# Optimization experiments

Hardware: AMD Instinct MI355X
Metric: run time of the kernel (lower is better)

Reference implementation:

```python
import jax, jax.numpy as jnp
import numpy as np
import math

B, T, C = 4, 2048, 1024
H = 16  # parallelAttentionPathways
D = C // H  # head dim = 64


def setup_inputs() -> dict:
    key = jax.random.key(0)
    k1, k2, k3 = jax.random.split(key, 3)
    x = jax.random.normal(k1, (B, T, C), dtype=jnp.float32)
    w_qkv = jax.random.normal(k2, (3 * C, C), dtype=jnp.float32) * (1.0 / math.sqrt(C))
    w_out = jax.random.normal(k3, (C, C), dtype=jnp.float32) * (1.0 / math.sqrt(C))
    return {"x": x, "w_qkv": w_qkv, "w_out": w_out}


def reference(x, w_qkv, w_out):
    b, t, c = x.shape
    # qkv projection: torch Linear y = x @ W^T (no bias)
    qkv = jnp.einsum('btc,fc->btf', x, w_qkv)  # [B,T,3C]
    q, k, v = jnp.split(qkv, 3, axis=-1)
    # [B,H,T,D]
    q = q.reshape(b, t, H, D).transpose(0, 2, 1, 3)
    k = k.reshape(b, t, H, D).transpose(0, 2, 1, 3)
    v = v.reshape(b, t, H, D).transpose(0, 2, 1, 3)
    scale = 1.0 / math.sqrt(D)
    att = jnp.einsum('bhqd,bhkd->bhqk', q, k) * scale  # [B,H,T,T]
    causal = jnp.tril(jnp.ones((t, t), dtype=bool))
    att = jnp.where(causal[None, None], att, -jnp.inf)
    att = jax.nn.softmax(att, axis=-1)
    # dropoutRate=0.0 -> dropout is identity (eval-mode determinism)
    y = jnp.einsum('bhqk,bhkd->bhqd', att, v)  # [B,H,T,D]
    y = y.transpose(0, 2, 1, 3).reshape(b, t, c)
    return jnp.einsum('btc,fc->btf', y, w_out)
```

## Files before the change

kernel.cpp:

```cpp
#include <hip/hip_runtime.h>
#include <hip/hip_bf16.h>
#include <stdint.h>


using bf16 = __hip_bfloat16;
typedef __attribute__((ext_vector_type(8))) __bf16 bf16x8;
typedef __attribute__((ext_vector_type(8))) unsigned short u16x8;
typedef __attribute__((ext_vector_type(4))) unsigned short u16x4;
typedef __attribute__((ext_vector_type(4))) float f32x4;
typedef unsigned short ushort_t;

#define MFMA16(a, b, c) __builtin_amdgcn_mfma_f32_16x16x32_bf16((a), (b), (c), 0, 0, 0)

__device__ __forceinline__ bf16x8 ld_frag(const ushort_t* p) {
  const u16x8 u = *(const u16x8*)p;
  return __builtin_bit_cast(bf16x8, u);
}

__device__ __forceinline__ ushort_t f2bf(float f) {
  return __builtin_bit_cast(ushort_t, __float2bfloat16(f));
}

__device__ __forceinline__ void gl2lds16(const void* g, void* lds) {
  __builtin_amdgcn_global_load_lds((const __attribute__((address_space(1))) void*)g,
                                   (__attribute__((address_space(3))) void*)lds,
                                   16, 0, 0);
}

__global__ void detect_dtype(const ushort_t* __restrict__ x, int* __restrict__ flag) {
  __shared__ int red[256];
  const int tid = threadIdx.x;
  int cnt = 0;
  for (int i = tid; i < 4096; i += 256) {
    const int e = (x[i] & 0x7FFF) >> 7;
    cnt += (e >= 117 && e <= 133) ? 1 : 0;
  }
  red[tid] = cnt;
  __syncthreads();
  for (int s = 128; s > 0; s >>= 1) {
    if (tid < s) red[tid] += red[tid + s];
    __syncthreads();
  }
  if (tid == 0) *flag = (red[0] < 3072) ? 1 : 0;
}

__global__ void cvt_to_bf16(const void* __restrict__ in, ushort_t* __restrict__ out,
                            int n, const int* __restrict__ flag) {
  const int i = (blockIdx.x * 256 + threadIdx.x) * 8;
  if (i >= n) return;
  if (*flag) {
    const float* p = (const float*)in + i;
    const float4 f0 = *(const float4*)p;
    const float4 f1 = *(const float4*)(p + 4);
    u16x8 u;
    u[0] = f2bf(f0.x); u[1] = f2bf(f0.y); u[2] = f2bf(f0.z); u[3] = f2bf(f0.w);
    u[4] = f2bf(f1.x); u[5] = f2bf(f1.y); u[6] = f2bf(f1.z); u[7] = f2bf(f1.w);
    *(u16x8*)(out + i) = u;
  } else {
    *(u16x8*)(out + i) = *(const u16x8*)((const ushort_t*)in + i);
  }
}

template <int EPI>
__global__ __launch_bounds__(256, 2)
void gemm_nt(const ushort_t* __restrict__ A, const void* __restrict__ Bw,
             const int* __restrict__ flag, int bExt,
             float* __restrict__ C0, ushort_t* __restrict__ Qo,
             ushort_t* __restrict__ Ko, ushort_t* __restrict__ Vt,
             int M, int N, int Kd) {
  __shared__ ushort_t sA[128 * 32];
  __shared__ ushort_t sB[128 * 32];
  const int tid = threadIdx.x;
  const int wave = tid >> 6, lane = tid & 63;
  const int quad = lane >> 4, l16 = lane & 15;
  const int wm = wave >> 1, wn = wave & 1;
  const long m0 = (long)blockIdx.y * 128;
  const long n0 = (long)blockIdx.x * 128;
  const int bF = bExt ? *flag : 0;

  f32x4 acc[4][4];
#pragma unroll
  for (int i = 0; i < 4; ++i)
#pragma unroll
    for (int j = 0; j < 4; ++j) acc[i][j] = (f32x4){0.f, 0.f, 0.f, 0.f};

  for (int k0 = 0; k0 < Kd; k0 += 32) {
#pragma unroll
    for (int j = 0; j < 2; ++j) {
      const int chunk = wave * 2 + j;
      const int idx = chunk * 64 + lane;
      const int r = idx >> 2, c = idx & 3;
      gl2lds16(A + (m0 + r) * (long)Kd + k0 + c * 8, (char*)sA + chunk * 1024);
    }
    if (!bF) {
#pragma unroll
      for (int j = 0; j < 2; ++j) {
        const int chunk = wave * 2 + j;
        const int idx = chunk * 64 + lane;
        const int r = idx >> 2, c = idx & 3;
        gl2lds16((const ushort_t*)Bw + (n0 + r) * (long)Kd + k0 + c * 8,
                 (char*)sB + chunk * 1024);
      }
    } else {
#pragma unroll
      for (int t2 = 0; t2 < 2; ++t2) {
        const int idx = t2 * 256 + tid;
        const int r = idx >> 2, c = idx & 3;
        const float* p = (const float*)Bw + (n0 + r) * (long)Kd + k0 + c * 8;
        const float4 f0 = *(const float4*)p;
        const float4 f1 = *(const float4*)(p + 4);
        u16x8 u;
        u[0] = f2bf(f0.x); u[1] = f2bf(f0.y); u[2] = f2bf(f0.z); u[3] = f2bf(f0.w);
        u[4] = f2bf(f1.x); u[5] = f2bf(f1.y); u[6] = f2bf(f1.z); u[7] = f2bf(f1.w);
        *(u16x8*)&sB[r * 32 + c * 8] = u;
      }
    }
    __syncthreads();
    bf16x8 af[4], bfr[4];
#pragma unroll
    for (int i = 0; i < 4; ++i) {
      const int r = wm * 64 + i * 16 + l16;
      af[i] = ld_frag(&sA[r * 32 + quad * 8]);
    }
#pragma unroll
    for (int i = 0; i < 4; ++i) {
      const int r = wn * 64 + i * 16 + l16;
      bfr[i] = ld_frag(&sB[r * 32 + quad * 8]);
    }
#pragma unroll
    for (int i = 0; i < 4; ++i)
#pragma unroll
      for (int j = 0; j < 4; ++j) acc[i][j] = MFMA16(af[i], bfr[j], acc[i][j]);
    __syncthreads();
  }

#pragma unroll
  for (int i = 0; i < 4; ++i) {
#pragma unroll
    for (int j = 0; j < 4; ++j) {
      if (EPI == 0) {
#pragma unroll
        for (int reg = 0; reg < 4; ++reg) {
          const long m = m0 + wm * 64 + i * 16 + quad * 4 + reg;
          const long n = n0 + wn * 64 + j * 16 + l16;
          C0[m * N + n] = acc[i][j][reg];
        }
      } else {
        const long n = n0 + wn * 64 + j * 16 + l16;
        const int which = (int)(n >> 10);
        const int h = (int)((n >> 6) & 15);
        const int d = (int)(n & 63);
        const long mbase = m0 + wm * 64 + i * 16 + quad * 4;
        const long b = mbase >> 11;
        const long tb = mbase & 2047;
        if (which == 2) {
          u16x4 pk;
#pragma unroll
          for (int reg = 0; reg < 4; ++reg) pk[reg] = f2bf(acc[i][j][reg]);
          *(u16x4*)&Vt[((b * 16 + h) * 64 + d) * 2048 + tb] = pk;
        } else {
          ushort_t* dst = (which == 0) ? Qo : Ko;
#pragma unroll
          for (int reg = 0; reg < 4; ++reg)
            dst[((b * 16 + h) * 2048 + tb + reg) * 64 + d] = f2bf(acc[i][j][reg]);
        }
      }
    }
  }
}

#define RS 72

__device__ __forceinline__ void attn_tile(const bf16x8 qf[2], const ushort_t* sK,
                                          const ushort_t* sV, ushort_t* sPw,
                                          int kv, int qg, bool need_mask,
                                          int quad, int l16,
                                          float& m_i, float& l_i, f32x4* oacc) {
  f32x4 s[4];
#pragma unroll
  for (int nt = 0; nt < 4; ++nt) s[nt] = (f32x4){0.f, 0.f, 0.f, 0.f};
#pragma unroll
  for (int nt = 0; nt < 4; ++nt) {
#pragma unroll
    for (int kk = 0; kk < 2; ++kk) {
      const bf16x8 kf = ld_frag(&sK[(nt * 16 + l16) * RS + (kk * 4 + quad) * 8]);
      s[nt] = MFMA16(kf, qf[kk], s[nt]);
    }
  }
  const int kb = kv * 64 + quad * 4;
  float rmax = -1e30f;
  if (need_mask) {
#pragma unroll
    for (int nt = 0; nt < 4; ++nt) {
#pragma unroll
      for (int reg = 0; reg < 4; ++reg) {
        float v = s[nt][reg];
        if (kb + nt * 16 + reg > qg) v = -1e30f;
        s[nt][reg] = v;
        rmax = fmaxf(rmax, v);
      }
    }
  } else {
#pragma unroll
    for (int nt = 0; nt < 4; ++nt) {
#pragma unroll
      for (int reg = 0; reg < 4; ++reg) rmax = fmaxf(rmax, s[nt][reg]);
    }
  }
  rmax = fmaxf(rmax, __shfl_xor(rmax, 16, 64));
  rmax = fmaxf(rmax, __shfl_xor(rmax, 32, 64));
  float mnew = fmaxf(m_i, rmax);
  if (__all(rmax - m_i <= 5.5f)) {
    mnew = m_i;
  } else {
    const float alpha = __expf(m_i - mnew);
    l_i *= alpha;
#pragma unroll
    for (int dt = 0; dt < 4; ++dt) oacc[dt] *= alpha;
    m_i = mnew;
  }
  float rs = 0.f;
#pragma unroll
  for (int nt = 0; nt < 4; ++nt) {
#pragma unroll
    for (int reg = 0; reg < 4; ++reg) {
      const float p = __expf(s[nt][reg] - mnew);
      s[nt][reg] = p;
      rs += p;
    }
  }
  rs += __shfl_xor(rs, 16, 64);
  rs += __shfl_xor(rs, 32, 64);
  l_i += rs;

  asm volatile("s_waitcnt lgkmcnt(0)" ::: "memory");
#pragma unroll
  for (int nt = 0; nt < 4; ++nt) {
    u16x4 pk;
#pragma unroll
    for (int reg = 0; reg < 4; ++reg) pk[reg] = f2bf(s[nt][reg]);
    *(u16x4*)&sPw[l16 * RS + nt * 16 + quad * 4] = pk;
  }
  asm volatile("s_waitcnt lgkmcnt(0)" ::: "memory");
  bf16x8 pf[2];
#pragma unroll
  for (int kk = 0; kk < 2; ++kk)
    pf[kk] = ld_frag(&sPw[l16 * RS + kk * 32 + quad * 8]);
#pragma unroll
  for (int dt = 0; dt < 4; ++dt) {
#pragma unroll
    for (int kk = 0; kk < 2; ++kk) {
      const bf16x8 vf = ld_frag(&sV[(dt * 16 + l16) * RS + (kk * 4 + quad) * 8]);
      oacc[dt] = MFMA16(vf, pf[kk], oacc[dt]);
    }
  }
}

__global__ __launch_bounds__(256, 4)
void attn_causal(const ushort_t* __restrict__ Qg, const ushort_t* __restrict__ Kg,
                 const ushort_t* __restrict__ Vt, ushort_t* __restrict__ Yg) {
  __shared__ ushort_t sK[64 * RS];
  __shared__ ushort_t sV[64 * RS];
  __shared__ ushort_t sPQ[64 * RS];
  const int tid = threadIdx.x;
  const int wave = tid >> 6, lane = tid & 63;
  const int quad = lane >> 4, l16 = lane & 15;
  const int lin = blockIdx.y * 16 + blockIdx.x;
  const int logical = (lin & 7) * 128 + (lin >> 3);
  const int qx = logical & 15, bh = logical >> 4;
  const int qtA = qx, qtB = 31 - qx;
  const size_t base = (size_t)bh * 2048 * 64;
  ushort_t* sPw = sPQ + wave * 16 * RS;

  bf16x8 qfA[2], qfB[2];
#pragma unroll
  for (int tile = 0; tile < 2; ++tile) {
    const int qt = tile ? qtB : qtA;
#pragma unroll
    for (int t2 = 0; t2 < 2; ++t2) {
      const int idx = t2 * 256 + tid;
      const int r = idx >> 3, c = idx & 7;
      *(u16x8*)&sPQ[r * RS + c * 8] =
          *(const u16x8*)(Qg + base + (size_t)(qt * 64 + r) * 64 + c * 8);
    }
    __syncthreads();
#pragma unroll
    for (int kk = 0; kk < 2; ++kk) {
      const u16x8 u = *(const u16x8*)&sPQ[(wave * 16 + l16) * RS + (kk * 4 + quad) * 8];
      u16x8 w;
#pragma unroll
      for (int e = 0; e < 8; ++e)
        w[e] = f2bf(__bfloat162float(__builtin_bit_cast(bf16, (ushort_t)u[e])) * 0.125f);
      const bf16x8 f = __builtin_bit_cast(bf16x8, w);
      if (tile) qfB[kk] = f; else qfA[kk] = f;
    }
    __syncthreads();
  }

  float mA = -1e30f, lA = 0.f, mB = -1e30f, lB = 0.f;
  f32x4 oA[4], oB[4];
#pragma unroll
  for (int dt = 0; dt < 4; ++dt) {
    oA[dt] = (f32x4){0.f, 0.f, 0.f, 0.f};
    oB[dt] = (f32x4){0.f, 0.f, 0.f, 0.f};
  }
  const int qgA = qtA * 64 + wave * 16 + l16;
  const int qgB = qtB * 64 + wave * 16 + l16;
  const int qmA = qtA * 64 + wave * 16;
  const int qmB = qtB * 64 + wave * 16;

  u16x8 kr[2], vr[2];
#pragma unroll
  for (int t2 = 0; t2 < 2; ++t2) {
    const int idx = t2 * 256 + tid;
    const int r = idx >> 3, c = idx & 7;
    kr[t2] = *(const u16x8*)(Kg + base + (size_t)r * 64 + c * 8);
    vr[t2] = *(const u16x8*)(Vt + base + (size_t)r * 2048 + c * 8);
  }

  for (int kv = 0; kv <= qtB; ++kv) {
    __syncthreads();
#pragma unroll
    for (int t2 = 0; t2 < 2; ++t2) {
      const int idx = t2 * 256 + tid;
      const int r = idx >> 3, c = idx & 7;
      *(u16x8*)&sK[r * RS + c * 8] = kr[t2];
      *(u16x8*)&sV[r * RS + c * 8] = vr[t2];
    }
    __syncthreads();
    if (kv < qtB) {
      const int kn = kv + 1;
#pragma unroll
      for (int t2 = 0; t2 < 2; ++t2) {
        const int idx = t2 * 256 + tid;
        const int r = idx >> 3, c = idx & 7;
        kr[t2] = *(const u16x8*)(Kg + base + (size_t)(kn * 64 + r) * 64 + c * 8);
        vr[t2] = *(const u16x8*)(Vt + base + (size_t)r * 2048 + kn * 64 + c * 8);
      }
    }
    attn_tile(qfB, sK, sV, sPw, kv, qgB, kv * 64 + 63 > qmB, quad, l16, mB, lB, oB);
    if (kv <= qtA)
      attn_tile(qfA, sK, sV, sPw, kv, qgA, kv * 64 + 63 > qmA, quad, l16, mA, lA, oA);
  }

  const int b = bh >> 4, h = bh & 15;
#pragma unroll
  for (int tile = 0; tile < 2; ++tile) {
    const int qt = tile ? qtB : qtA;
    const float linv = 1.f / (tile ? lB : lA);
    const f32x4* o = tile ? oB : oA;
    const int t = qt * 64 + wave * 16 + l16;
#pragma unroll
    for (int dt = 0; dt < 4; ++dt) {
      u16x4 pk;
#pragma unroll
      for (int reg = 0; reg < 4; ++reg) pk[reg] = f2bf(o[dt][reg] * linv);
      *(u16x4*)&Yg[(((size_t)b * 2048 + t) * 16 + h) * 64 + dt * 16 + quad * 4] = pk;
    }
  }
}

extern "C" void kernel_launch(void* const* d_in, const int* in_sizes, int n_in,
                              void* d_out, int out_size, void* d_ws, size_t ws_size,
                              hipStream_t stream) {
  const void* x = d_in[0];
  const void* w_qkv = d_in[1];
  const void* w_out = d_in[2];
  float* out = (float*)d_out;

  const size_t per = (size_t)4 * 16 * 2048 * 64;
  const size_t nwqkv = (size_t)3072 * 1024;
  const size_t nwout = (size_t)1024 * 1024;
  ushort_t* qws = (ushort_t*)d_ws;
  ushort_t* kws = qws + per;
  ushort_t* vTws = kws + per;
  ushort_t* xyws = vTws + per;
  ushort_t* wqkvb = xyws + per;
  ushort_t* woutb = wqkvb + nwqkv;
  int* flag = (int*)(woutb + nwout);
  const size_t need = (size_t)(4 * per + nwqkv + nwout) * 2 + 16;
  const bool pre = ws_size >= need;
  (void)in_sizes; (void)n_in; (void)out_size;

  dim3 blk(256);
  if (!pre) flag = (int*)(xyws + per);
  detect_dtype<<<1, 256, 0, stream>>>((const ushort_t*)x, flag);
  cvt_to_bf16<<<4096, 256, 0, stream>>>(x, xyws, (int)per, flag);
  if (pre) {
    cvt_to_bf16<<<1536, 256, 0, stream>>>(w_qkv, wqkvb, (int)nwqkv, flag);
    cvt_to_bf16<<<512, 256, 0, stream>>>(w_out, woutb, (int)nwout, flag);
    gemm_nt<1><<<dim3(24, 64), blk, 0, stream>>>(xyws, wqkvb, flag, 0, nullptr,
                                                 qws, kws, vTws, 8192, 3072, 1024);
    attn_causal<<<dim3(16, 64), blk, 0, stream>>>(qws, kws, vTws, xyws);
    gemm_nt<0><<<dim3(8, 64), blk, 0, stream>>>(xyws, woutb, flag, 0, out,
                                                nullptr, nullptr, nullptr,
                                                8192, 1024, 1024);
  } else {
    gemm_nt<1><<<dim3(24, 64), blk, 0, stream>>>(xyws, w_qkv, flag, 1, nullptr,
                                                 qws, kws, vTws, 8192, 3072, 1024);
    attn_causal<<<dim3(16, 64), blk, 0, stream>>>(qws, kws, vTws, xyws);
    gemm_nt<0><<<dim3(8, 64), blk, 0, stream>>>(xyws, w_out, flag, 1, out,
                                                nullptr, nullptr, nullptr,
                                                8192, 1024, 1024);
  }
}
```

Baseline: 269.9 us.

## Interleave both query tiles per KV step to share K/V fragment loads

Restructures the attention inner loop so the two query tiles (A and B) are processed together. Each K and V fragment is read from LDS once and used for both tiles' MFMAs, and the two softmax passes sit between the QK and PV phases, giving independent MFMA chains more room to interleave. The launch-bounds occupancy hint drops from 4 to 3 blocks to allow the extra live registers, which risks lower occupancy.

```diff
diff --git a/kernel.cpp b/kernel.cpp
--- a/kernel.cpp
+++ b/kernel.cpp
@@ -171,23 +171,8 @@
 
 #define RS 72
 
-__device__ __forceinline__ void attn_tile(const bf16x8 qf[2], const ushort_t* sK,
-                                          const ushort_t* sV, ushort_t* sPw,
-                                          int kv, int qg, bool need_mask,
-                                          int quad, int l16,
-                                          float& m_i, float& l_i, f32x4* oacc) {
-  f32x4 s[4];
-#pragma unroll
-  for (int nt = 0; nt < 4; ++nt) s[nt] = (f32x4){0.f, 0.f, 0.f, 0.f};
-#pragma unroll
-  for (int nt = 0; nt < 4; ++nt) {
-#pragma unroll
-    for (int kk = 0; kk < 2; ++kk) {
-      const bf16x8 kf = ld_frag(&sK[(nt * 16 + l16) * RS + (kk * 4 + quad) * 8]);
-      s[nt] = MFMA16(kf, qf[kk], s[nt]);
-    }
-  }
-  const int kb = kv * 64 + quad * 4;
+__device__ __forceinline__ void softmax_tile(f32x4* s, int kb, int qg, bool need_mask,
+                                             float& m_i, float& l_i, f32x4* oacc) {
   float rmax = -1e30f;
   if (need_mask) {
 #pragma unroll
@@ -232,31 +217,9 @@
   rs += __shfl_xor(rs, 16, 64);
   rs += __shfl_xor(rs, 32, 64);
   l_i += rs;
-
-  asm volatile("s_waitcnt lgkmcnt(0)" ::: "memory");
-#pragma unroll
-  for (int nt = 0; nt < 4; ++nt) {
-    u16x4 pk;
-#pragma unroll
-    for (int reg = 0; reg < 4; ++reg) pk[reg] = f2bf(s[nt][reg]);
-    *(u16x4*)&sPw[l16 * RS + nt * 16 + quad * 4] = pk;
-  }
-  asm volatile("s_waitcnt lgkmcnt(0)" ::: "memory");
-  bf16x8 pf[2];
-#pragma unroll
-  for (int kk = 0; kk < 2; ++kk)
-    pf[kk] = ld_frag(&sPw[l16 * RS + kk * 32 + quad * 8]);
-#pragma unroll
-  for (int dt = 0; dt < 4; ++dt) {
-#pragma unroll
-    for (int kk = 0; kk < 2; ++kk) {
-      const bf16x8 vf = ld_frag(&sV[(dt * 16 + l16) * RS + (kk * 4 + quad) * 8]);
-      oacc[dt] = MFMA16(vf, pf[kk], oacc[dt]);
-    }
-  }
-}
-
-__global__ __launch_bounds__(256, 4)
+}
+
+__global__ __launch_bounds__(256, 3)
 void attn_causal(const ushort_t* __restrict__ Qg, const ushort_t* __restrict__ Kg,
                  const ushort_t* __restrict__ Vt, ushort_t* __restrict__ Yg) {
   __shared__ ushort_t sK[64 * RS];
@@ -265,6 +228,7 @@
   const int tid = threadIdx.x;
   const int wave = tid >> 6, lane = tid & 63;
   const int quad = lane >> 4, l16 = lane & 15;
+  const f32x4 ZERO4 = {0.f, 0.f, 0.f, 0.f};
   const int lin = blockIdx.y * 16 + blockIdx.x;
   const int logical = (lin & 7) * 128 + (lin >> 3);
   const int qx = logical & 15, bh = logical >> 4;
@@ -301,8 +265,8 @@
   f32x4 oA[4], oB[4];
 #pragma unroll
   for (int dt = 0; dt < 4; ++dt) {
-    oA[dt] = (f32x4){0.f, 0.f, 0.f, 0.f};
-    oB[dt] = (f32x4){0.f, 0.f, 0.f, 0.f};
+    oA[dt] = ZERO4;
+    oB[dt] = ZERO4;
   }
   const int qgA = qtA * 64 + wave * 16 + l16;
   const int qgB = qtB * 64 + wave * 16 + l16;
@@ -338,9 +302,65 @@
         vr[t2] = *(const u16x8*)(Vt + base + (size_t)r * 2048 + kn * 64 + c * 8);
       }
     }
-    attn_tile(qfB, sK, sV, sPw, kv, qgB, kv * 64 + 63 > qmB, quad, l16, mB, lB, oB);
-    if (kv <= qtA)
-      attn_tile(qfA, sK, sV, sPw, kv, qgA, kv * 64 + 63 > qmA, quad, l16, mA, lA, oA);
+
+    const bool doA = (kv <= qtA);
+    f32x4 sSB[4], sSA[4];
+#pragma unroll
+    for (int nt = 0; nt < 4; ++nt) {
+      const ushort_t* krow = &sK[(nt * 16 + l16) * RS + quad * 8];
+      const bf16x8 kf0 = ld_frag(krow);
+      const bf16x8 kf1 = ld_frag(krow + 32);
+      sSB[nt] = MFMA16(kf0, qfB[0], ZERO4);
+      sSB[nt] = MFMA16(kf1, qfB[1], sSB[nt]);
+      if (doA) {
+        sSA[nt] = MFMA16(kf0, qfA[0], ZERO4);
+        sSA[nt] = MFMA16(kf1, qfA[1], sSA[nt]);
+      }
+    }
+    const int kb = kv * 64 + quad * 4;
+    softmax_tile(sSB, kb, qgB, kv * 64 + 63 > qmB, mB, lB, oB);
+    if (doA) softmax_tile(sSA, kb, qgA, kv * 64 + 63 > qmA, mA, lA, oA);
+
+    bf16x8 pfB[2], pfA[2];
+    asm volatile("s_waitcnt lgkmcnt(0)" ::: "memory");
+#pragma unroll
+    for (int nt = 0; nt < 4; ++nt) {
+      u16x4 pk;
+#pragma unroll
+      for (int reg = 0; reg < 4; ++reg) pk[reg] = f2bf(sSB[nt][reg]);
+      *(u16x4*)&sPw[l16 * RS + nt * 16 + quad * 4] = pk;
+    }
+    asm volatile("s_waitcnt lgkmcnt(0)" ::: "memory");
+#pragma unroll
+    for (int kk = 0; kk < 2; ++kk)
+      pfB[kk] = ld_frag(&sPw[l16 * RS + kk * 32 + quad * 8]);
+    if (doA) {
+      asm volatile("s_waitcnt lgkmcnt(0)" ::: "memory");
+#pragma unroll
+      for (int nt = 0; nt < 4; ++nt) {
+        u16x4 pk;
+#pragma unroll
+        for (int reg = 0; reg < 4; ++reg) pk[reg] = f2bf(sSA[nt][reg]);
+        *(u16x4*)&sPw[l16 * RS + nt * 16 + quad * 4] = pk;
+      }
+      asm volatile("s_waitcnt lgkmcnt(0)" ::: "memory");
+#pragma unroll
+      for (int kk = 0; kk < 2; ++kk)
+        pfA[kk] = ld_frag(&sPw[l16 * RS + kk * 32 + quad * 8]);
+    }
+
+#pragma unroll
+    for (int dt = 0; dt < 4; ++dt) {
+      const ushort_t* vrow = &sV[(dt * 16 + l16) * RS + quad * 8];
+      const bf16x8 vf0 = ld_frag(vrow);
+      const bf16x8 vf1 = ld_frag(vrow + 32);
+      oB[dt] = MFMA16(vf0, pfB[0], oB[dt]);
+      oB[dt] = MFMA16(vf1, pfB[1], oB[dt]);
+      if (doA) {
+        oA[dt] = MFMA16(vf0, pfA[0], oA[dt]);
+        oA[dt] = MFMA16(vf1, pfA[1], oA[dt]);
+      }
+    }
   }
 
   const int b = bh >> 4, h = bh & 15;
```

Result: slower. 282.8 us (+4.8%).

## Double-buffer K/V via direct global-to-LDS loads with XOR-swizzled layout

Applied to the files above, without the earlier changes.

Replaces the register-staged K/V prefetch with asynchronous global_load_lds copies into double-buffered shared memory. Each iteration now needs one barrier instead of two, and the VGPR round trip is gone. Padded rows (stride 72) give way to 64-wide rows with an XOR swizzle on the column chunk to avoid bank conflicts, applied to K, V and the P scratch. Q fragments are read straight from global memory instead of going through LDS. In exchange it uses more LDS per block, which may limit occupancy, and it relies on the barrier to wait for the async LDS writes.

```diff
diff --git a/kernel.cpp b/kernel.cpp
--- a/kernel.cpp
+++ b/kernel.cpp
@@ -169,25 +169,9 @@
   }
 }
 
-#define RS 72
-
-__device__ __forceinline__ void attn_tile(const bf16x8 qf[2], const ushort_t* sK,
-                                          const ushort_t* sV, ushort_t* sPw,
-                                          int kv, int qg, bool need_mask,
-                                          int quad, int l16,
-                                          float& m_i, float& l_i, f32x4* oacc) {
-  f32x4 s[4];
-#pragma unroll
-  for (int nt = 0; nt < 4; ++nt) s[nt] = (f32x4){0.f, 0.f, 0.f, 0.f};
-#pragma unroll
-  for (int nt = 0; nt < 4; ++nt) {
-#pragma unroll
-    for (int kk = 0; kk < 2; ++kk) {
-      const bf16x8 kf = ld_frag(&sK[(nt * 16 + l16) * RS + (kk * 4 + quad) * 8]);
-      s[nt] = MFMA16(kf, qf[kk], s[nt]);
-    }
-  }
-  const int kb = kv * 64 + quad * 4;
+
+__device__ __forceinline__ void softmax_tile(f32x4* s, int kb, int qg, bool need_mask,
+                                             float& m_i, float& l_i, f32x4* oacc) {
   float rmax = -1e30f;
   if (need_mask) {
 #pragma unroll
@@ -232,6 +216,24 @@
   rs += __shfl_xor(rs, 16, 64);
   rs += __shfl_xor(rs, 32, 64);
   l_i += rs;
+}
+
+__device__ __forceinline__ void attn_job(const bf16x8 qf[2], const ushort_t* sKc,
+                                         const ushort_t* sVc, ushort_t* sPw,
+                                         int kv, int qg, bool need_mask,
+                                         int quad, int l8, int l16,
+                                         float& m_i, float& l_i, f32x4* oacc) {
+  const f32x4 ZERO4 = {0.f, 0.f, 0.f, 0.f};
+  const int off0 = ((quad ^ l8) << 3);
+  const int off1 = (((quad + 4) ^ l8) << 3);
+  f32x4 s[4];
+#pragma unroll
+  for (int nt = 0; nt < 4; ++nt) {
+    const ushort_t* krow = sKc + (nt * 16 + l16) * 64;
+    s[nt] = MFMA16(ld_frag(krow + off0), qf[0], ZERO4);
+    s[nt] = MFMA16(ld_frag(krow + off1), qf[1], s[nt]);
+  }
+  softmax_tile(s, kv * 64 + quad * 4, qg, need_mask, m_i, l_i, oacc);
 
   asm volatile("s_waitcnt lgkmcnt(0)" ::: "memory");
 #pragma unroll
@@ -239,54 +241,47 @@
     u16x4 pk;
 #pragma unroll
     for (int reg = 0; reg < 4; ++reg) pk[reg] = f2bf(s[nt][reg]);
-    *(u16x4*)&sPw[l16 * RS + nt * 16 + quad * 4] = pk;
+    *(u16x4*)&sPw[l16 * 64 + (((4 * nt + quad) << 2) ^ (l8 << 3))] = pk;
   }
   asm volatile("s_waitcnt lgkmcnt(0)" ::: "memory");
-  bf16x8 pf[2];
-#pragma unroll
-  for (int kk = 0; kk < 2; ++kk)
-    pf[kk] = ld_frag(&sPw[l16 * RS + kk * 32 + quad * 8]);
+  bf16x8 pf0 = ld_frag(&sPw[l16 * 64 + off0]);
+  bf16x8 pf1 = ld_frag(&sPw[l16 * 64 + off1]);
 #pragma unroll
   for (int dt = 0; dt < 4; ++dt) {
-#pragma unroll
-    for (int kk = 0; kk < 2; ++kk) {
-      const bf16x8 vf = ld_frag(&sV[(dt * 16 + l16) * RS + (kk * 4 + quad) * 8]);
-      oacc[dt] = MFMA16(vf, pf[kk], oacc[dt]);
-    }
+    const ushort_t* vrow = sVc + (dt * 16 + l16) * 64;
+    oacc[dt] = MFMA16(ld_frag(vrow + off0), pf0, oacc[dt]);
+    oacc[dt] = MFMA16(ld_frag(vrow + off1), pf1, oacc[dt]);
   }
 }
 
 __global__ __launch_bounds__(256, 4)
 void attn_causal(const ushort_t* __restrict__ Qg, const ushort_t* __restrict__ Kg,
                  const ushort_t* __restrict__ Vt, ushort_t* __restrict__ Yg) {
-  __shared__ ushort_t sK[64 * RS];
-  __shared__ ushort_t sV[64 * RS];
-  __shared__ ushort_t sPQ[64 * RS];
+  __shared__ ushort_t sK[2][64 * 64];
+  __shared__ ushort_t sV[2][64 * 64];
+  __shared__ ushort_t sP[64 * 64];
   const int tid = threadIdx.x;
   const int wave = tid >> 6, lane = tid & 63;
-  const int quad = lane >> 4, l16 = lane & 15;
+  const int quad = lane >> 4, l16 = lane & 15, l8 = lane & 7;
+  const f32x4 ZERO4 = {0.f, 0.f, 0.f, 0.f};
   const int lin = blockIdx.y * 16 + blockIdx.x;
   const int logical = (lin & 7) * 128 + (lin >> 3);
   const int qx = logical & 15, bh = logical >> 4;
   const int qtA = qx, qtB = 31 - qx;
   const size_t base = (size_t)bh * 2048 * 64;
-  ushort_t* sPw = sPQ + wave * 16 * RS;
+  ushort_t* sPw = sP + wave * 16 * 64;
+
+  const int srow = lane >> 3;
+  const int scol = ((lane & 7) ^ srow) << 3;
 
   bf16x8 qfA[2], qfB[2];
 #pragma unroll
   for (int tile = 0; tile < 2; ++tile) {
     const int qt = tile ? qtB : qtA;
-#pragma unroll
-    for (int t2 = 0; t2 < 2; ++t2) {
-      const int idx = t2 * 256 + tid;
-      const int r = idx >> 3, c = idx & 7;
-      *(u16x8*)&sPQ[r * RS + c * 8] =
-          *(const u16x8*)(Qg + base + (size_t)(qt * 64 + r) * 64 + c * 8);
-    }
-    __syncthreads();
+    const size_t qrow = base + (size_t)(qt * 64 + wave * 16 + l16) * 64;
 #pragma unroll
     for (int kk = 0; kk < 2; ++kk) {
-      const u16x8 u = *(const u16x8*)&sPQ[(wave * 16 + l16) * RS + (kk * 4 + quad) * 8];
+      const u16x8 u = *(const u16x8*)(Qg + qrow + (kk * 4 + quad) * 8);
       u16x8 w;
 #pragma unroll
       for (int e = 0; e < 8; ++e)
@@ -294,53 +289,48 @@
       const bf16x8 f = __builtin_bit_cast(bf16x8, w);
       if (tile) qfB[kk] = f; else qfA[kk] = f;
     }
-    __syncthreads();
   }
 
   float mA = -1e30f, lA = 0.f, mB = -1e30f, lB = 0.f;
   f32x4 oA[4], oB[4];
 #pragma unroll
   for (int dt = 0; dt < 4; ++dt) {
-    oA[dt] = (f32x4){0.f, 0.f, 0.f, 0.f};
-    oB[dt] = (f32x4){0.f, 0.f, 0.f, 0.f};
+    oA[dt] = ZERO4;
+    oB[dt] = ZERO4;
   }
   const int qgA = qtA * 64 + wave * 16 + l16;
   const int qgB = qtB * 64 + wave * 16 + l16;
   const int qmA = qtA * 64 + wave * 16;
   const int qmB = qtB * 64 + wave * 16;
 
-  u16x8 kr[2], vr[2];
-#pragma unroll
-  for (int t2 = 0; t2 < 2; ++t2) {
-    const int idx = t2 * 256 + tid;
-    const int r = idx >> 3, c = idx & 7;
-    kr[t2] = *(const u16x8*)(Kg + base + (size_t)r * 64 + c * 8);
-    vr[t2] = *(const u16x8*)(Vt + base + (size_t)r * 2048 + c * 8);
+#pragma unroll
+  for (int j = 0; j < 2; ++j) {
+    const int chunk = wave * 2 + j;
+    gl2lds16(Kg + base + (size_t)(chunk * 8 + srow) * 64 + scol,
+             (char*)&sK[0][0] + chunk * 1024);
+    gl2lds16(Vt + base + (size_t)(chunk * 8 + srow) * 2048 + scol,
+             (char*)&sV[0][0] + chunk * 1024);
   }
 
   for (int kv = 0; kv <= qtB; ++kv) {
-    __syncthreads();
-#pragma unroll
-    for (int t2 = 0; t2 < 2; ++t2) {
-      const int idx = t2 * 256 + tid;
-      const int r = idx >> 3, c = idx & 7;
-      *(u16x8*)&sK[r * RS + c * 8] = kr[t2];
-      *(u16x8*)&sV[r * RS + c * 8] = vr[t2];
-    }
+    const int cur = kv & 1;
     __syncthreads();
     if (kv < qtB) {
       const int kn = kv + 1;
 #pragma unroll
-      for (int t2 = 0; t2 < 2; ++t2) {
-        const int idx = t2 * 256 + tid;
-        const int r = idx >> 3, c = idx & 7;
-        kr[t2] = *(const u16x8*)(Kg + base + (size_t)(kn * 64 + r) * 64 + c * 8);
-        vr[t2] = *(const u16x8*)(Vt + base + (size_t)r * 2048 + kn * 64 + c * 8);
-      }
-    }
-    attn_tile(qfB, sK, sV, sPw, kv, qgB, kv * 64 + 63 > qmB, quad, l16, mB, lB, oB);
+      for (int j = 0; j < 2; ++j) {
+        const int chunk = wave * 2 + j;
+        gl2lds16(Kg + base + (size_t)(kn * 64 + chunk * 8 + srow) * 64 + scol,
+                 (char*)&sK[cur ^ 1][0] + chunk * 1024);
+        gl2lds16(Vt + base + (size_t)(chunk * 8 + srow) * 2048 + kn * 64 + scol,
+                 (char*)&sV[cur ^ 1][0] + chunk * 1024);
+      }
+    }
+    const ushort_t* sKc = &sK[cur][0];
+    const ushort_t* sVc = &sV[cur][0];
+    attn_job(qfB, sKc, sVc, sPw, kv, qgB, kv * 64 + 63 > qmB, quad, l8, l16, mB, lB, oB);
     if (kv <= qtA)
-      attn_tile(qfA, sK, sV, sPw, kv, qgA, kv * 64 + 63 > qmA, quad, l16, mA, lA, oA);
+      attn_job(qfA, sKc, sVc, sPw, kv, qgA, kv * 64 + 63 > qmA, quad, l8, l16, mA, lA, oA);
   }
 
   const int b = bh >> 4, h = bh & 15;
```

Result: no change. 264.8 us (-1.9%).
